# Optimization experiments

Measured on AMD Instinct MI355X. Metric: run time of the kernel, lower is better.

The kernel has to match this reference:

```python
import jax, jax.numpy as jnp
import numpy as np

B, T, E = 4, 2048, 1024
H, KV = 16, 4          # query heads, key/value heads
D = E // H             # head_dim = 64
G = H // KV            # query heads per kv head = 4
NEG = -1e9


def setup_inputs() -> dict:
    key = jax.random.key(0)
    ks = jax.random.split(key, 6)
    hidden_states = jax.random.normal(ks[0], (B, T, E), dtype=jnp.float32)
    # additive causal mask [B, 1, T, T]
    causal = jnp.where(jnp.tril(jnp.ones((T, T), dtype=bool)), 0.0, NEG).astype(jnp.float32)
    attention_mask = jnp.broadcast_to(causal[None, None], (B, 1, T, T))
    s = 0.02
    Wq = jax.random.normal(ks[1], (E, E), dtype=jnp.float32) * s
    Wk = jax.random.normal(ks[2], (E, KV * D), dtype=jnp.float32) * s
    Wv = jax.random.normal(ks[3], (E, KV * D), dtype=jnp.float32) * s
    Wo = jax.random.normal(ks[4], (E, E), dtype=jnp.float32) * s
    bq = jnp.zeros((E,), jnp.float32)
    bk = jnp.zeros((KV * D,), jnp.float32)
    bv = jnp.zeros((KV * D,), jnp.float32)
    bo = jnp.zeros((E,), jnp.float32)
    return {"hidden_states": hidden_states, "attention_mask": attention_mask,
            "Wq": Wq, "bq": bq, "Wk": Wk, "bk": bk, "Wv": Wv, "bv": bv,
            "Wo": Wo, "bo": bo}


def reference(hidden_states, attention_mask, Wq, bq, Wk, bk, Wv, bv, Wo, bo):
    b, t, e = hidden_states.shape
    scaling = D ** -0.5
    # projections (torch Linear: x @ W + b with W stored [in, out])
    q = (hidden_states @ Wq + bq) * scaling           # [b, t, E]
    k = hidden_states @ Wk + bk                        # [b, t, KV*D]
    v = hidden_states @ Wv + bv
    # [b, KV, G, t, D] for q; [b, KV, t, D] for k/v (GQA grouping == repeat_kv math)
    q = q.reshape(b, t, KV, G, D).transpose(0, 2, 3, 1, 4)
    k = k.reshape(b, t, KV, D).transpose(0, 2, 1, 3)
    v = v.reshape(b, t, KV, D).transpose(0, 2, 1, 3)
    scores = jnp.einsum('bkgsd,bktd->bkgst', q, k)     # [b, KV, G, t, t]
    scores = scores + attention_mask[:, :, None, :, :]  # broadcast [b,1,1,t,t]
    w = jax.nn.softmax(scores, axis=-1)
    out = jnp.einsum('bkgst,bktd->bkgsd', w, v)        # [b, KV, G, t, D]
    out = out.transpose(0, 3, 1, 2, 4).reshape(b, t, e)  # heads back to embed
    return out @ Wo + bo
```

## Files before the change

kernel.cpp:

```cpp
#include <hip/hip_runtime.h>

typedef __bf16 bf16;
typedef __attribute__((ext_vector_type(8))) __bf16 bf16x8;
typedef __attribute__((ext_vector_type(4))) __bf16 bf16x4;
typedef __attribute__((ext_vector_type(2))) __bf16 bf16x2;
typedef __attribute__((ext_vector_type(4))) float f32x4;
typedef __attribute__((ext_vector_type(4))) unsigned u32x4;

#define B_ 4
#define T_ 2048
#define E_ 1024
#define H_ 16
#define KV_ 4
#define D_ 64
#define KVD_ 256
#define QKVS_ 1536
#define M_ 8192

#define MASK_NEG (-3.0e4f)
#define QSCALE (0.125f * 1.4426950408889634f)

__device__ inline bf16x8 load8(const bf16* p) { return *(const bf16x8*)p; }
__device__ inline bf16x8 load8(const float* p) {
  f32x4 a = *(const f32x4*)p;
  f32x4 b = *(const f32x4*)(p + 4);
  bf16x8 r;
#pragma unroll
  for (int j = 0; j < 4; ++j) { r[j] = (bf16)a[j]; r[4 + j] = (bf16)b[j]; }
  return r;
}

__device__ inline void gload_lds16(const bf16* g, bf16* l) {
  __builtin_amdgcn_global_load_lds(
      (const __attribute__((address_space(1))) void*)g,
      (__attribute__((address_space(3))) void*)l, 16, 0, 0);
}

__device__ inline float fexp2(float x) {
#if __has_builtin(__builtin_amdgcn_exp2f)
  return __builtin_amdgcn_exp2f(x);
#else
  float r;
  asm("v_exp_f32 %0, %1" : "=v"(r) : "v"(x));
  return r;
#endif
}

__device__ inline unsigned pk2(float a, float b) {
  bf16x2 t; t[0] = (bf16)a; t[1] = (bf16)b;
  return __builtin_bit_cast(unsigned, t);
}

__device__ inline void plswap32(unsigned& x, unsigned& y) {
#if __has_builtin(__builtin_amdgcn_permlane32_swap)
  auto r = __builtin_amdgcn_permlane32_swap((int)x, (int)y, false, false);
  x = (unsigned)r[0]; y = (unsigned)r[1];
#else
  asm volatile("v_permlane32_swap_b32 %0, %1" : "+v"(x), "+v"(y));
#endif
}

__device__ inline void plswap16(unsigned& x, unsigned& y) {
#if __has_builtin(__builtin_amdgcn_permlane16_swap)
  auto r = __builtin_amdgcn_permlane16_swap((int)x, (int)y, false, false);
  x = (unsigned)r[0]; y = (unsigned)r[1];
#else
  asm volatile("v_permlane16_swap_b32 %0, %1" : "+v"(x), "+v"(y));
#endif
}

__global__ __launch_bounds__(256) void prep_k(const float* __restrict__ hidden,
                                              bf16* __restrict__ Hb,
                                              const float* __restrict__ Wq,
                                              const float* __restrict__ Wk,
                                              const float* __restrict__ Wv,
                                              const float* __restrict__ Wo,
                                              bf16* __restrict__ WqkvT,
                                              bf16* __restrict__ WoT) {
  const int z = blockIdx.z;
  if (z >= 4) {
    size_t lin = (size_t)blockIdx.x + 32 * blockIdx.y + 1024 * (z - 4);
    size_t i = lin * 2048 + (size_t)threadIdx.x * 8;
    *(bf16x8*)(Hb + i) = load8(hidden + i);
    return;
  }
  const float* W;
  bf16* WT;
  int N;
  if (z == 0) { W = Wq; WT = WqkvT; N = 1024; }
  else if (z == 1) { W = Wo; WT = WoT; N = 1024; }
  else if (z == 2) { if (blockIdx.y >= 8) return; W = Wk; WT = WqkvT + 1024 * 1024; N = 256; }
  else { if (blockIdx.y >= 8) return; W = Wv; WT = WqkvT + 1280 * 1024; N = 256; }

  __shared__ bf16 tile[32][33];
  int k0 = blockIdx.x * 32, n0 = blockIdx.y * 32;
  int tr = threadIdx.x >> 5;
  int tc = threadIdx.x & 31;
#pragma unroll
  for (int i = 0; i < 32; i += 8)
    tile[tr + i][tc] = (bf16)W[(size_t)(k0 + tr + i) * N + n0 + tc];
  __syncthreads();
#pragma unroll
  for (int i = 0; i < 32; i += 8)
    WT[(size_t)(n0 + tr + i) * 1024 + k0 + tc] = tile[tc][tr + i];
}

__global__ __launch_bounds__(256) void vtrans_k(const bf16* __restrict__ src,
                                                bf16* __restrict__ dst) {
  __shared__ bf16 tile[32][33];
  int r0 = blockIdx.x * 32;
  int c0 = blockIdx.y * 32;
  int tr = threadIdx.x >> 5, tc = threadIdx.x & 31;
#pragma unroll
  for (int i = 0; i < 32; i += 8)
    tile[tr + i][tc] = src[(size_t)(r0 + tr + i) * QKVS_ + 1280 + c0 + tc];
  __syncthreads();
#pragma unroll
  for (int i = 0; i < 32; i += 8) {
    int c = c0 + tr + i;
    int r = r0 + tc;
    dst[(size_t)((r >> 11) * KVD_ + c) * T_ + (r & (T_ - 1))] = tile[tc][tr + i];
  }
}

__global__ __launch_bounds__(256) void qkv_gemm_k(const bf16* __restrict__ A,
                                                  const bf16* __restrict__ WT,
                                                  const float* __restrict__ bq,
                                                  const float* __restrict__ bk,
                                                  const float* __restrict__ bv,
                                                  bf16* __restrict__ C) {
  const int K = E_;
  const int m0 = blockIdx.x * 128;
  const int n0 = blockIdx.y * 128;
  const int tid = threadIdx.x;
  const int wave = tid >> 6;
  const int lane = tid & 63;
  const int wr = wave >> 1;
  const int wc = wave & 1;
  const int fr = lane & 15;
  const int quad = lane >> 4;

  __shared__ bf16 sA[2][128][32];
  __shared__ bf16 sB[2][128][32];

  f32x4 acc[4][4] = {};

  const int ldr = lane >> 2;
  const int ldk = (lane & 3) * 8;
  const bf16* Ag0 = A + (size_t)(m0 + wave * 32 + ldr) * K + ldk;
  const bf16* Ag1 = Ag0 + (size_t)16 * K;
  const bf16* Bg0 = WT + (size_t)(n0 + wave * 32 + ldr) * K + ldk;
  const bf16* Bg1 = Bg0 + (size_t)16 * K;

  gload_lds16(Ag0, &sA[0][wave * 32][0]);
  gload_lds16(Ag1, &sA[0][wave * 32 + 16][0]);
  gload_lds16(Bg0, &sB[0][wave * 32][0]);
  gload_lds16(Bg1, &sB[0][wave * 32 + 16][0]);
  __syncthreads();

  for (int k0 = 0; k0 < K; k0 += 32) {
    const int cur = (k0 >> 5) & 1;
    if (k0 + 32 < K) {
      const int nxt = cur ^ 1;
      gload_lds16(Ag0 + k0 + 32, &sA[nxt][wave * 32][0]);
      gload_lds16(Ag1 + k0 + 32, &sA[nxt][wave * 32 + 16][0]);
      gload_lds16(Bg0 + k0 + 32, &sB[nxt][wave * 32][0]);
      gload_lds16(Bg1 + k0 + 32, &sB[nxt][wave * 32 + 16][0]);
    }

    bf16x8 af[4], bfr[4];
#pragma unroll
    for (int m = 0; m < 4; ++m)
      af[m] = *(const bf16x8*)(&sA[cur][wr * 64 + m * 16 + fr][quad * 8]);
#pragma unroll
    for (int n = 0; n < 4; ++n)
      bfr[n] = *(const bf16x8*)(&sB[cur][wc * 64 + n * 16 + fr][quad * 8]);
#pragma unroll
    for (int m = 0; m < 4; ++m)
#pragma unroll
      for (int n = 0; n < 4; ++n)
        acc[m][n] = __builtin_amdgcn_mfma_f32_16x16x32_bf16(af[m], bfr[n], acc[m][n], 0, 0, 0);
    __syncthreads();
  }

#pragma unroll
  for (int n = 0; n < 4; ++n) {
    int col = n0 + wc * 64 + n * 16 + fr;
    float bias, sc;
    if (col < 1024) { bias = bq[col]; sc = QSCALE; }
    else if (col < 1280) { bias = bk[col - 1024]; sc = 1.f; }
    else { bias = bv[col - 1280]; sc = 1.f; }
#pragma unroll
    for (int m = 0; m < 4; ++m) {
#pragma unroll
      for (int i = 0; i < 4; ++i) {
        int row = m0 + wr * 64 + m * 16 + quad * 4 + i;
        C[(size_t)row * QKVS_ + col] = (bf16)((acc[m][n][i] + bias) * sc);
      }
    }
  }
}

__global__ __launch_bounds__(256) void gemm128_k(const bf16* __restrict__ A,
                                                 const bf16* __restrict__ WT,
                                                 const float* __restrict__ bias,
                                                 float* __restrict__ C,
                                                 int M, int N, int K) {
  const int m0 = blockIdx.x * 128;
  const int n0 = blockIdx.y * 128;
  const int tid = threadIdx.x;
  const int wave = tid >> 6;
  const int lane = tid & 63;
  const int wr = wave >> 1;
  const int wc = wave & 1;
  const int fr = lane & 15;
  const int quad = lane >> 4;

  __shared__ bf16 sA[2][128][32];
  __shared__ bf16 sB[2][128][32];

  f32x4 acc[4][4] = {};

  const int ldr = lane >> 2;
  const int ldk = (lane & 3) * 8;
  const bf16* Ag0 = A + (size_t)(m0 + wave * 32 + ldr) * K + ldk;
  const bf16* Ag1 = Ag0 + (size_t)16 * K;
  const bf16* Bg0 = WT + (size_t)(n0 + wave * 32 + ldr) * K + ldk;
  const bf16* Bg1 = Bg0 + (size_t)16 * K;

  gload_lds16(Ag0, &sA[0][wave * 32][0]);
  gload_lds16(Ag1, &sA[0][wave * 32 + 16][0]);
  gload_lds16(Bg0, &sB[0][wave * 32][0]);
  gload_lds16(Bg1, &sB[0][wave * 32 + 16][0]);
  __syncthreads();

  for (int k0 = 0; k0 < K; k0 += 32) {
    const int cur = (k0 >> 5) & 1;
    if (k0 + 32 < K) {
      const int nxt = cur ^ 1;
      gload_lds16(Ag0 + k0 + 32, &sA[nxt][wave * 32][0]);
      gload_lds16(Ag1 + k0 + 32, &sA[nxt][wave * 32 + 16][0]);
      gload_lds16(Bg0 + k0 + 32, &sB[nxt][wave * 32][0]);
      gload_lds16(Bg1 + k0 + 32, &sB[nxt][wave * 32 + 16][0]);
    }

    bf16x8 af[4], bfr[4];
#pragma unroll
    for (int m = 0; m < 4; ++m)
      af[m] = *(const bf16x8*)(&sA[cur][wr * 64 + m * 16 + fr][quad * 8]);
#pragma unroll
    for (int n = 0; n < 4; ++n)
      bfr[n] = *(const bf16x8*)(&sB[cur][wc * 64 + n * 16 + fr][quad * 8]);
#pragma unroll
    for (int m = 0; m < 4; ++m)
#pragma unroll
      for (int n = 0; n < 4; ++n)
        acc[m][n] = __builtin_amdgcn_mfma_f32_16x16x32_bf16(af[m], bfr[n], acc[m][n], 0, 0, 0);
    __syncthreads();
  }

#pragma unroll
  for (int n = 0; n < 4; ++n) {
    int col = n0 + wc * 64 + n * 16 + fr;
    float bv = bias[col];
#pragma unroll
    for (int m = 0; m < 4; ++m) {
#pragma unroll
      for (int i = 0; i < 4; ++i) {
        int row = m0 + wr * 64 + m * 16 + quad * 4 + i;
        C[(size_t)row * N + col] = (acc[m][n][i] + bv);
      }
    }
  }
}

__global__ __launch_bounds__(256) void attn_k(const bf16* __restrict__ QKVg,
                                              const bf16* __restrict__ VTg,
                                              bf16* __restrict__ Og) {
  const int jp = blockIdx.x;
  const int h = blockIdx.y;
  const int b = blockIdx.z;
  const int kv = h >> 2;
  const int tid = threadIdx.x;
  const int wave = tid >> 6;
  const int lane = tid & 63;
  const int fr = lane & 15;
  const int quad = lane >> 4;

  __shared__ bf16 Ks[64][72];
  __shared__ bf16 Vt[64][72];

  const int skey = tid & 63;
  const int sdc = (tid >> 6) * 16;
  const int svd = tid >> 2;
  const int svk = (tid & 3) * 16;
  const bf16* kbase = QKVg + (size_t)(b * T_ + skey) * QKVS_ + 1024 + kv * 64 + sdc;
  const bf16* vbase = VTg + (size_t)((b * KV_ + kv) * D_ + svd) * T_ + svk;

  for (int ph = 0; ph < 2; ++ph) {
    const int qb = ph ? (31 - jp) : jp;

    bf16x8 qa0, qa1;
    {
      const bf16* qsrc = QKVg + (size_t)(b * T_ + qb * 64 + wave * 16 + fr) * QKVS_ + h * 64 + quad * 8;
      qa0 = *(const bf16x8*)(qsrc);
      qa1 = *(const bf16x8*)(qsrc + 32);
    }

    f32x4 Oacc[4] = {};
    float l_part = 0.f;

    bf16x8 k0p, k1p, v0p, v1p;
    k0p = *(const bf16x8*)(kbase);
    k1p = *(const bf16x8*)(kbase + 8);
    v0p = *(const bf16x8*)(vbase);
    v1p = *(const bf16x8*)(vbase + 8);

    for (int kb = 0; kb <= qb; ++kb) {
      *(bf16x8*)(&Ks[skey][sdc]) = k0p;
      *(bf16x8*)(&Ks[skey][sdc + 8]) = k1p;
      *(bf16x8*)(&Vt[svd][svk]) = v0p;
      *(bf16x8*)(&Vt[svd][svk + 8]) = v1p;
      __syncthreads();

      if (kb < qb) {
        const bf16* kp = kbase + (size_t)(kb + 1) * 64 * QKVS_;
        const bf16* vp = vbase + (size_t)(kb + 1) * 64;
        k0p = *(const bf16x8*)(kp);
        k1p = *(const bf16x8*)(kp + 8);
        v0p = *(const bf16x8*)(vp);
        v1p = *(const bf16x8*)(vp + 8);
      } else if (ph == 0) {
        k0p = *(const bf16x8*)(kbase);
        k1p = *(const bf16x8*)(kbase + 8);
        v0p = *(const bf16x8*)(vbase);
        v1p = *(const bf16x8*)(vbase + 8);
      }

      f32x4 S[4] = {};
      __builtin_amdgcn_s_setprio(1);
#pragma unroll
      for (int nt = 0; nt < 4; ++nt) {
        bf16x8 kf0 = *(const bf16x8*)(&Ks[nt * 16 + fr][quad * 8]);
        bf16x8 kf1 = *(const bf16x8*)(&Ks[nt * 16 + fr][32 + quad * 8]);
        S[nt] = __builtin_amdgcn_mfma_f32_16x16x32_bf16(kf0, qa0, S[nt], 0, 0, 0);
        S[nt] = __builtin_amdgcn_mfma_f32_16x16x32_bf16(kf1, qa1, S[nt], 0, 0, 0);
      }
      __builtin_amdgcn_s_setprio(0);

      if (kb == qb) {
        const int ql = wave * 16 + fr;
#pragma unroll
        for (int nt = 0; nt < 4; ++nt)
#pragma unroll
          for (int i = 0; i < 4; ++i)
            if (nt * 16 + quad * 4 + i > ql) S[nt][i] = MASK_NEG;
      }

#pragma unroll
      for (int nt = 0; nt < 4; ++nt)
#pragma unroll
        for (int i = 0; i < 4; ++i) {
          float p = fexp2(S[nt][i]);
          S[nt][i] = p;
          l_part += p;
        }

      bf16x8 pb0, pb1;
      {
        unsigned d00 = pk2(S[0][0], S[0][1]), d01 = pk2(S[0][2], S[0][3]);
        unsigned d10 = pk2(S[1][0], S[1][1]), d11 = pk2(S[1][2], S[1][3]);
        unsigned d20 = pk2(S[2][0], S[2][1]), d21 = pk2(S[2][2], S[2][3]);
        unsigned d30 = pk2(S[3][0], S[3][1]), d31 = pk2(S[3][2], S[3][3]);
        plswap32(d00, d10); plswap16(d00, d10);
        plswap32(d01, d11); plswap16(d01, d11);
        plswap32(d20, d30); plswap16(d20, d30);
        plswap32(d21, d31); plswap16(d21, d31);
        u32x4 f0, f1;
        f0[0] = d00; f0[1] = d01; f0[2] = d10; f0[3] = d11;
        f1[0] = d20; f1[1] = d21; f1[2] = d30; f1[3] = d31;
        pb0 = __builtin_bit_cast(bf16x8, f0);
        pb1 = __builtin_bit_cast(bf16x8, f1);
      }

      __builtin_amdgcn_s_setprio(1);
#pragma unroll
      for (int dt = 0; dt < 4; ++dt) {
        bf16x8 vf0 = *(const bf16x8*)(&Vt[dt * 16 + fr][quad * 8]);
        bf16x8 vf1 = *(const bf16x8*)(&Vt[dt * 16 + fr][32 + quad * 8]);
        Oacc[dt] = __builtin_amdgcn_mfma_f32_16x16x32_bf16(vf0, pb0, Oacc[dt], 0, 0, 0);
        Oacc[dt] = __builtin_amdgcn_mfma_f32_16x16x32_bf16(vf1, pb1, Oacc[dt], 0, 0, 0);
      }
      __builtin_amdgcn_s_setprio(0);
      __syncthreads();
    }

    {
      float l = l_part;
      l += __shfl_xor(l, 16, 64);
      l += __shfl_xor(l, 32, 64);
      float inv = 1.f / fmaxf(l, 1e-30f);
      bf16* dst = Og + (size_t)(b * T_ + qb * 64 + wave * 16 + fr) * E_ + h * 64;
#pragma unroll
      for (int dt = 0; dt < 4; ++dt) {
        bf16x4 o;
#pragma unroll
        for (int i = 0; i < 4; ++i) o[i] = (bf16)(Oacc[dt][i] * inv);
        *(bf16x4*)(dst + dt * 16 + quad * 4) = o;
      }
    }
  }
}

extern "C" void kernel_launch(void* const* d_in, const int* in_sizes, int n_in,
                              void* d_out, int out_size, void* d_ws, size_t ws_size,
                              hipStream_t stream) {
  (void)in_sizes; (void)n_in; (void)out_size; (void)ws_size;
  const float* hidden = (const float*)d_in[0];
  const float* Wq = (const float*)d_in[2];
  const float* bq = (const float*)d_in[3];
  const float* Wk = (const float*)d_in[4];
  const float* bk = (const float*)d_in[5];
  const float* Wv = (const float*)d_in[6];
  const float* bv = (const float*)d_in[7];
  const float* Wo = (const float*)d_in[8];
  const float* bo = (const float*)d_in[9];
  float* out = (float*)d_out;

  char* ws = (char*)d_ws;
  bf16* WqkvT = (bf16*)(ws);
  bf16* WoT   = (bf16*)(ws + (3u << 20));
  bf16* QKVb  = (bf16*)(ws + (5u << 20));
  bf16* Hb    = (bf16*)(ws + (29u << 20));
  bf16* Ab    = (bf16*)(ws + (29u << 20));
  bf16* VbT   = (bf16*)(ws + (45u << 20));

  prep_k<<<dim3(32, 32, 8), 256, 0, stream>>>(hidden, Hb, Wq, Wk, Wv, Wo, WqkvT, WoT);

  qkv_gemm_k<<<dim3(64, 12), 256, 0, stream>>>(Hb, WqkvT, bq, bk, bv, QKVb);

  vtrans_k<<<dim3(256, 8), 256, 0, stream>>>(QKVb, VbT);

  attn_k<<<dim3(16, 16, 4), 256, 0, stream>>>(QKVb, VbT, Ab);

  gemm128_k<<<dim3(64, 8), 256, 0, stream>>>(Ab, WoT, bo, out, M_, E_, E_);
}
```

Measured before the change: 268.4 us.

## Use 128-row query tiles with 512-thread blocks in causal attention

The attention kernel now processes 128 query rows per block using 8 waves (512 threads) instead of 64 rows with 4 waves, halving the grid. Each K/V tile staged in shared memory is reused by twice as many query rows, and each thread loads one 8-element segment instead of two. The causal masking now covers the last two 64-key tiles relative to the 128-row query block. The risk is fewer blocks in the grid and more wasted work on the diagonal tiles, since the first half of the query rows compute a fully masked key tile.

```diff
diff --git a/kernel.cpp b/kernel.cpp
--- a/kernel.cpp
+++ b/kernel.cpp
@@ -274,7 +274,7 @@
   }
 }
 
-__global__ __launch_bounds__(256) void attn_k(const bf16* __restrict__ QKVg,
+__global__ __launch_bounds__(512) void attn_k(const bf16* __restrict__ QKVg,
                                               const bf16* __restrict__ VTg,
                                               bf16* __restrict__ Og) {
   const int jp = blockIdx.x;
@@ -290,19 +290,18 @@
   __shared__ bf16 Ks[64][72];
   __shared__ bf16 Vt[64][72];
 
-  const int skey = tid & 63;
-  const int sdc = (tid >> 6) * 16;
-  const int svd = tid >> 2;
-  const int svk = (tid & 3) * 16;
-  const bf16* kbase = QKVg + (size_t)(b * T_ + skey) * QKVS_ + 1024 + kv * 64 + sdc;
-  const bf16* vbase = VTg + (size_t)((b * KV_ + kv) * D_ + svd) * T_ + svk;
+  const int srow = tid & 63;
+  const int sseg = (tid >> 6) * 8;
+  const bf16* kbase = QKVg + (size_t)(b * T_ + srow) * QKVS_ + 1024 + kv * 64 + sseg;
+  const bf16* vbase = VTg + (size_t)((b * KV_ + kv) * D_ + srow) * T_ + sseg;
 
   for (int ph = 0; ph < 2; ++ph) {
-    const int qb = ph ? (31 - jp) : jp;
+    const int qb = ph ? (15 - jp) : jp;
+    const int kmax = 2 * qb + 1;
 
     bf16x8 qa0, qa1;
     {
-      const bf16* qsrc = QKVg + (size_t)(b * T_ + qb * 64 + wave * 16 + fr) * QKVS_ + h * 64 + quad * 8;
+      const bf16* qsrc = QKVg + (size_t)(b * T_ + qb * 128 + wave * 16 + fr) * QKVS_ + h * 64 + quad * 8;
       qa0 = *(const bf16x8*)(qsrc);
       qa1 = *(const bf16x8*)(qsrc + 32);
     }
@@ -310,31 +309,21 @@
     f32x4 Oacc[4] = {};
     float l_part = 0.f;
 
-    bf16x8 k0p, k1p, v0p, v1p;
-    k0p = *(const bf16x8*)(kbase);
-    k1p = *(const bf16x8*)(kbase + 8);
-    v0p = *(const bf16x8*)(vbase);
-    v1p = *(const bf16x8*)(vbase + 8);
-
-    for (int kb = 0; kb <= qb; ++kb) {
-      *(bf16x8*)(&Ks[skey][sdc]) = k0p;
-      *(bf16x8*)(&Ks[skey][sdc + 8]) = k1p;
-      *(bf16x8*)(&Vt[svd][svk]) = v0p;
-      *(bf16x8*)(&Vt[svd][svk + 8]) = v1p;
+    bf16x8 kp_, vp_;
+    kp_ = *(const bf16x8*)(kbase);
+    vp_ = *(const bf16x8*)(vbase);
+
+    for (int kb = 0; kb <= kmax; ++kb) {
+      *(bf16x8*)(&Ks[srow][sseg]) = kp_;
+      *(bf16x8*)(&Vt[srow][sseg]) = vp_;
       __syncthreads();
 
-      if (kb < qb) {
-        const bf16* kp = kbase + (size_t)(kb + 1) * 64 * QKVS_;
-        const bf16* vp = vbase + (size_t)(kb + 1) * 64;
-        k0p = *(const bf16x8*)(kp);
-        k1p = *(const bf16x8*)(kp + 8);
-        v0p = *(const bf16x8*)(vp);
-        v1p = *(const bf16x8*)(vp + 8);
+      if (kb < kmax) {
+        kp_ = *(const bf16x8*)(kbase + (size_t)(kb + 1) * 64 * QKVS_);
+        vp_ = *(const bf16x8*)(vbase + (size_t)(kb + 1) * 64);
       } else if (ph == 0) {
-        k0p = *(const bf16x8*)(kbase);
-        k1p = *(const bf16x8*)(kbase + 8);
-        v0p = *(const bf16x8*)(vbase);
-        v1p = *(const bf16x8*)(vbase + 8);
+        kp_ = *(const bf16x8*)(kbase);
+        vp_ = *(const bf16x8*)(vbase);
       }
 
       f32x4 S[4] = {};
@@ -348,13 +337,14 @@
       }
       __builtin_amdgcn_s_setprio(0);
 
-      if (kb == qb) {
+      if (kb >= 2 * qb) {
+        const int kgb = (kb - 2 * qb) * 64;
         const int ql = wave * 16 + fr;
 #pragma unroll
         for (int nt = 0; nt < 4; ++nt)
 #pragma unroll
           for (int i = 0; i < 4; ++i)
-            if (nt * 16 + quad * 4 + i > ql) S[nt][i] = MASK_NEG;
+            if (kgb + nt * 16 + quad * 4 + i > ql) S[nt][i] = MASK_NEG;
       }
 
 #pragma unroll
@@ -400,7 +390,7 @@
       l += __shfl_xor(l, 16, 64);
       l += __shfl_xor(l, 32, 64);
       float inv = 1.f / fmaxf(l, 1e-30f);
-      bf16* dst = Og + (size_t)(b * T_ + qb * 64 + wave * 16 + fr) * E_ + h * 64;
+      bf16* dst = Og + (size_t)(b * T_ + qb * 128 + wave * 16 + fr) * E_ + h * 64;
 #pragma unroll
       for (int dt = 0; dt < 4; ++dt) {
         bf16x4 o;
@@ -441,7 +431,7 @@
 
   vtrans_k<<<dim3(256, 8), 256, 0, stream>>>(QKVb, VbT);
 
-  attn_k<<<dim3(16, 16, 4), 256, 0, stream>>>(QKVb, VbT, Ab);
+  attn_k<<<dim3(8, 16, 4), 512, 0, stream>>>(QKVb, VbT, Ab);
 
   gemm128_k<<<dim3(64, 8), 256, 0, stream>>>(Ab, WoT, bo, out, M_, E_, E_);
 }
```

Measured after the change: 259.2 us. 1.04x faster.
